# Kernel tuning notes

Measured on AMD Instinct MI355X. Metric: run time of the kernel, lower is better.

The kernel has to match this reference:

```python
import jax, jax.numpy as jnp
import numpy as np

B, T, V, E, H, L = 64, 512, 50000, 256, 256, 9


def _lstm_dir(x, w_ih, w_hh, b, reverse):
    # x: [B,T,I]; w_ih: [4H,I]; w_hh: [4H,H]; b: [4H]. PyTorch gate order i,f,g,o.
    Bm, Hm = x.shape[0], w_hh.shape[1]
    gx = jnp.einsum('bti,gi->btg', x, w_ih) + b  # [B,T,4H] precomputed input proj

    def step(carry, g_t):
        h, c = carry
        gates = g_t + h @ w_hh.T
        i, f, g, o = jnp.split(gates, 4, axis=-1)
        c = jax.nn.sigmoid(f) * c + jax.nn.sigmoid(i) * jnp.tanh(g)
        h = jax.nn.sigmoid(o) * jnp.tanh(c)
        return (h, c), h

    init = (jnp.zeros((Bm, Hm), x.dtype), jnp.zeros((Bm, Hm), x.dtype))
    _, hs = jax.lax.scan(step, init, jnp.swapaxes(gx, 0, 1), reverse=reverse)
    return jnp.swapaxes(hs, 0, 1)  # [B,T,H]


def _bilstm_layer(x, w_ih, w_hh, b):
    fwd = _lstm_dir(x, w_ih[0], w_hh[0], b[0], False)
    bwd = _lstm_dir(x, w_ih[1], w_hh[1], b[1], True)
    return jnp.concatenate([fwd, bwd], axis=-1)  # [B,T,2H]


def _crf_nll(emissions, labels, mask, trans, start_trans, end_trans):
    # emissions: [B,T,L]; labels: [B,T] int; mask: [B,T] (mask[:,0] assumed 1)
    maskf = mask.astype(emissions.dtype)
    # gold path score
    em_lab = jnp.take_along_axis(emissions, labels[..., None], axis=2)[..., 0]  # [B,T]
    trans_sc = trans[labels[:, :-1], labels[:, 1:]]  # [B,T-1]
    score = start_trans[labels[:, 0]] + em_lab[:, 0] \
        + jnp.sum((trans_sc + em_lab[:, 1:]) * maskf[:, 1:], axis=1)
    last_idx = jnp.sum(mask, axis=1).astype(jnp.int32) - 1
    last_lab = jnp.take_along_axis(labels, last_idx[:, None].astype(labels.dtype), axis=1)[:, 0]
    score = score + end_trans[last_lab]
    # log-partition via forward algorithm (scan over time)
    alpha0 = start_trans[None, :] + emissions[:, 0]  # [B,L]

    def step(alpha, xs):
        em_t, m_t = xs
        new = jax.nn.logsumexp(alpha[:, :, None] + trans[None], axis=1) + em_t
        alpha = jnp.where(m_t[:, None] > 0, new, alpha)
        return alpha, None

    alpha, _ = jax.lax.scan(
        step, alpha0,
        (jnp.swapaxes(emissions[:, 1:], 0, 1), jnp.swapaxes(mask[:, 1:], 0, 1)))
    logZ = jax.nn.logsumexp(alpha + end_trans[None, :], axis=1)  # [B]
    return -(score - logZ).mean()


def setup_inputs() -> dict:
    key = jax.random.key(0)
    ks = jax.random.split(key, 16)
    s = 0.05
    inp = {
        'input_ids': jax.random.randint(ks[0], (B, T), 0, V),
        'attention_mask': jnp.ones((B, T), jnp.int32),
        'labels': jax.random.randint(ks[1], (B, T), 0, L),
        'emb': jax.random.normal(ks[2], (V, E), jnp.float32) * s,
        # layer 0: input size E; layer 1: input size 2H. [dir, 4H, in]
        'w_ih0': jax.random.normal(ks[3], (2, 4 * H, E), jnp.float32) * s,
        'w_hh0': jax.random.normal(ks[4], (2, 4 * H, H), jnp.float32) * s,
        'b0': jax.random.normal(ks[5], (2, 4 * H), jnp.float32) * s,
        'w_ih1': jax.random.normal(ks[6], (2, 4 * H, 2 * H), jnp.float32) * s,
        'w_hh1': jax.random.normal(ks[7], (2, 4 * H, H), jnp.float32) * s,
        'b1': jax.random.normal(ks[8], (2, 4 * H), jnp.float32) * s,
        'lin_w': jax.random.normal(ks[9], (L, 2 * H), jnp.float32) * s,
        'lin_b': jax.random.normal(ks[10], (L,), jnp.float32) * s,
        'trans': jax.random.normal(ks[11], (L, L), jnp.float32) * 0.1,
        'start_trans': jax.random.normal(ks[12], (L,), jnp.float32) * 0.1,
        'end_trans': jax.random.normal(ks[13], (L,), jnp.float32) * 0.1,
    }
    return inp


def reference(input_ids, attention_mask, labels, emb, w_ih0, w_hh0, b0,
              w_ih1, w_hh1, b1, lin_w, lin_b, trans, start_trans, end_trans):
    x = emb[input_ids]                       # [B,T,E]
    x = _bilstm_layer(x, w_ih0, w_hh0, b0)   # [B,T,2H]
    x = _bilstm_layer(x, w_ih1, w_hh1, b1)   # [B,T,2H]
    emissions = x @ lin_w.T + lin_b          # [B,T,L]
    loss = _crf_nll(emissions, labels, attention_mask, trans, start_trans, end_trans)
    return loss
```

## Files before the change

### kernel.cpp

```cpp
#include <hip/hip_runtime.h>
#include <stdint.h>
#include <stddef.h>

#define B_ 64
#define T_ 512
#define E_ 256
#define H_ 256
#define L_ 9
#define BT (B_*T_)
#define G4 1024
#define N2 2048

typedef short    bf16x8  __attribute__((ext_vector_type(8)));
typedef float    f32x4   __attribute__((ext_vector_type(4)));
typedef int      i32x8   __attribute__((ext_vector_type(8)));

__device__ __forceinline__ unsigned short f2bf(float x){
    unsigned u = __builtin_bit_cast(unsigned, x);
    u += 0x7fffu + ((u >> 16) & 1u);
    return (unsigned short)(u >> 16);
}
__device__ __forceinline__ float bf2f(unsigned short h){
    unsigned u = ((unsigned)h) << 16;
    return __builtin_bit_cast(float, u);
}

__device__ __forceinline__ unsigned char f32_e4m3(float x){
    unsigned b = __builtin_bit_cast(unsigned, x);
    unsigned s = b >> 31;
    float a = fabsf(x);
    if (a >= 448.f) return (unsigned char)((s<<7) | 0x7E);
    int E = (int)((b>>23)&255) - 127;
    if (E < -6) E = -6;
    int qi = (int)rintf(a * exp2f((float)(3 - E)));
    if (qi >= 16){ qi >>= 1; ++E; }
    if (qi == 0) return (unsigned char)(s<<7);
    unsigned mag = (qi >= 8) ? ((((unsigned)(E + 7)) << 3) | (unsigned)(qi - 8))
                             : (unsigned)qi;
    return (unsigned char)((s<<7) | mag);
}

__device__ __forceinline__ float sigm(float x){
    return __builtin_amdgcn_rcpf(1.f + __expf(-x));
}
__device__ __forceinline__ float tanh_(float x){
    float e = __expf(2.f*x);
    return 1.f - 2.f*__builtin_amdgcn_rcpf(e + 1.f);
}

__device__ __forceinline__ void lds_load16(void* lds, const void* g){
    __builtin_amdgcn_global_load_lds(
        (const __attribute__((address_space(1))) void*)g,
        (__attribute__((address_space(3))) void*)lds, 16, 0, 0);
}

__device__ __forceinline__ void store_out(unsigned short* p, float v){ *p = f2bf(v); }
__device__ __forceinline__ void store_out(float* p, float v){ *p = v; }

__global__ void k_embed(const int* __restrict__ ids, const float* __restrict__ emb,
                        unsigned short* __restrict__ x0){
    int bt = blockIdx.x;
    int e  = threadIdx.x;
    int id = ids[bt];
    x0[(size_t)bt*E_ + e] = f2bf(emb[(size_t)id*E_ + e]);
}

__global__ void k_pack_wih(const float* __restrict__ in, unsigned short* __restrict__ out, int K){
    int p = blockIdx.y;
    int k = blockIdx.x*256 + threadIdx.x;
    int dirc = p >> 10, pp = p & 1023;
    int wv = pp >> 7, rem = pp & 127;
    int uh = (rem >> 6) & 1, g = (rem >> 4) & 3, ulx = rem & 15;
    int orig = dirc*1024 + g*256 + wv*32 + uh*16 + ulx;
    out[(size_t)p*K + k] = f2bf(in[(size_t)orig*K + k]);
}

__global__ void k_pack_bias(const float* __restrict__ b, float* __restrict__ bp){
    int p = blockIdx.x*256 + threadIdx.x;
    int dirc = p >> 10, pp = p & 1023;
    int wv = pp >> 7, rem = pp & 127;
    int uh = (rem >> 6) & 1, g = (rem >> 4) & 3, ulx = rem & 15;
    int orig = dirc*1024 + g*256 + wv*32 + uh*16 + ulx;
    bp[p] = b[orig];
}

__global__ void k_pack_wfp8(const float* __restrict__ whh, unsigned char* __restrict__ wpk){
    int idx = blockIdx.x*256 + threadIdx.x;
    int lane = idx & 63;
    int uh   = (idx >> 6) & 1;
    int g    = (idx >> 7) & 3;
    int kt   = (idx >> 9) & 1;
    int wv   = (idx >> 10) & 7;
    int dir  = (idx >> 13) & 1;
    int ulx = lane & 15, hi4 = lane >> 4;
    int row = g*256 + wv*32 + uh*16 + ulx;
    int k0 = kt*128 + hi4*32;
    const float* src = whh + ((size_t)dir*G4 + row)*H_ + k0;
    unsigned char* dst = wpk + (size_t)idx*32;
    #pragma unroll
    for (int q = 0; q < 32; ++q) dst[q] = f32_e4m3(src[q]);
}

__global__ __launch_bounds__(256) void k_gemm(const unsigned short* __restrict__ A,
                                              const unsigned short* __restrict__ Bm,
                                              const float* __restrict__ bias,
                                              unsigned short* __restrict__ C,
                                              int M, int N, int K){
    __shared__ unsigned short As[128*32];
    __shared__ unsigned short Bs[128*32];
    int tid = threadIdx.x, lane = tid & 63, w = tid >> 6;
    int wm = w >> 1, wn = w & 1;
    int tileM = blockIdx.y * 128, tileN = blockIdx.x * 128;
    f32x4 acc[4][4] = {};
    const char* Ab = (const char*)A;
    const char* Bb = (const char*)Bm;
    for (int k0 = 0; k0 < K; k0 += 32){
        #pragma unroll
        for (int i = 0; i < 2; ++i){
            int off = (w*2 + i)*1024 + lane*16;
            int row = off >> 6, colb = off & 63;
            lds_load16((char*)As + (w*2+i)*1024,
                       Ab + ((size_t)(tileM + row)*K + k0)*2 + colb);
            lds_load16((char*)Bs + (w*2+i)*1024,
                       Bb + ((size_t)(tileN + row)*K + k0)*2 + colb);
        }
        __syncthreads();
        int kloc = (lane >> 4) * 8;
        bf16x8 af[4], bfv[4];
        #pragma unroll
        for (int mf = 0; mf < 4; ++mf)
            af[mf] = *(const bf16x8*)&As[(wm*64 + mf*16 + (lane & 15))*32 + kloc];
        #pragma unroll
        for (int nf = 0; nf < 4; ++nf)
            bfv[nf] = *(const bf16x8*)&Bs[(wn*64 + nf*16 + (lane & 15))*32 + kloc];
        #pragma unroll
        for (int mf = 0; mf < 4; ++mf)
            #pragma unroll
            for (int nf = 0; nf < 4; ++nf)
                acc[mf][nf] = __builtin_amdgcn_mfma_f32_16x16x32_bf16(
                                  af[mf], bfv[nf], acc[mf][nf], 0, 0, 0);
        __syncthreads();
    }
    #pragma unroll
    for (int mf = 0; mf < 4; ++mf){
        #pragma unroll
        for (int nf = 0; nf < 4; ++nf){
            int row0 = tileM + wm*64 + mf*16 + (lane >> 4)*4;
            int col  = tileN + wn*64 + nf*16 + (lane & 15);
            float bv = bias[col];
            #pragma unroll
            for (int r = 0; r < 4; ++r)
                C[(size_t)(row0 + r)*N + col] = f2bf(acc[mf][nf][r] + bv);
        }
    }
}

template<typename OutT>
__global__ __launch_bounds__(512, 2)
void k_rec_mfma(const unsigned short* __restrict__ gx,
                const unsigned char* __restrict__ wpk,
                OutT* __restrict__ out){
    int blk = blockIdx.x;
    int dir = blk & 1, bg = blk >> 1;
    int tid = threadIdx.x, lane = tid & 63, w = tid >> 6;
    int ul = lane & 15, hi4 = lane >> 4;
    int batch = bg*4 + hi4;

    __shared__ __align__(16) unsigned char hlds[2][32][16][8];
    {
        unsigned long long* hz = (unsigned long long*)hlds;
        for (int i = tid; i < 1024; i += 512) hz[i] = 0ull;
    }

    i32x8 wf[2][4][2];
    {
        const i32x8* wb = (const i32x8*)wpk;
        #pragma unroll
        for (int kt = 0; kt < 2; ++kt)
            #pragma unroll
            for (int g = 0; g < 4; ++g)
                #pragma unroll
                for (int uh = 0; uh < 2; ++uh)
                    wf[kt][g][uh] = wb[((((size_t)(dir*8 + w)*2 + kt)*4 + g)*2 + uh)*64 + lane];
    }
    __syncthreads();

    const unsigned short* gp = gx + (size_t)(batch*T_ + (dir ? T_-1 : 0))*N2
                                  + dir*1024 + w*128 + ul;
    ptrdiff_t dstep = dir ? -(ptrdiff_t)N2 : (ptrdiff_t)N2;

    unsigned short gxr[8];
    #pragma unroll
    for (int uh = 0; uh < 2; ++uh)
        #pragma unroll
        for (int g = 0; g < 4; ++g)
            gxr[uh*4+g] = gp[uh*64 + g*16];

    float c0 = 0.f, c1 = 0.f;
    int u0 = w*32 + ul, u1 = u0 + 16;
    OutT* ob = out + (size_t)batch*T_*512 + dir*256;

    for (int s = 0; s < T_; ++s){
        int buf = s & 1;
        f32x4 acc[4][2];
        #pragma unroll
        for (int g = 0; g < 4; ++g)
            #pragma unroll
            for (int uh = 0; uh < 2; ++uh)
                acc[g][uh] = (f32x4){ bf2f(gxr[uh*4+g]), 0.f, 0.f, 0.f };

        gp += dstep;
        unsigned short gxn[8];
        #pragma unroll
        for (int uh = 0; uh < 2; ++uh)
            #pragma unroll
            for (int g = 0; g < 4; ++g)
                gxn[uh*4+g] = gp[uh*64 + g*16];

        const unsigned long long* hrow = (const unsigned long long*)&hlds[buf][0][0][0];
        #pragma unroll
        for (int kt = 0; kt < 2; ++kt){
            unsigned long long a0 = hrow[(kt*16 + hi4*4 + 0)*16 + ul];
            unsigned long long a1 = hrow[(kt*16 + hi4*4 + 1)*16 + ul];
            unsigned long long a2 = hrow[(kt*16 + hi4*4 + 2)*16 + ul];
            unsigned long long a3 = hrow[(kt*16 + hi4*4 + 3)*16 + ul];
            i32x8 af = (i32x8){ (int)a0, (int)(a0>>32), (int)a1, (int)(a1>>32),
                                (int)a2, (int)(a2>>32), (int)a3, (int)(a3>>32) };
            #pragma unroll
            for (int g = 0; g < 4; ++g)
                #pragma unroll
                for (int uh = 0; uh < 2; ++uh)
                    acc[g][uh] = __builtin_amdgcn_mfma_scale_f32_16x16x128_f8f6f4(
                                     af, wf[kt][g][uh], acc[g][uh],
                                     0, 0,
                                     0, 0x7f7f7f7f,
                                     0, 0x7f7f7f7f);
        }

        int tt = dir ? (T_-1-s) : s;
        float h0, h1;
        {
            float xi = acc[0][0][0], xf = acc[1][0][0], xg = acc[2][0][0], xo = acc[3][0][0];
            c0 = sigm(xf)*c0 + sigm(xi)*tanh_(xg);
            h0 = sigm(xo)*tanh_(c0);
        }
        {
            float xi = acc[0][1][0], xf = acc[1][1][0], xg = acc[2][1][0], xo = acc[3][1][0];
            c1 = sigm(xf)*c1 + sigm(xi)*tanh_(xg);
            h1 = sigm(xo)*tanh_(c1);
        }

        unsigned char hb0, hb1;
#if __has_builtin(__builtin_amdgcn_cvt_pk_fp8_f32)
        {
            int pk = __builtin_amdgcn_cvt_pk_fp8_f32(h0, h1, 0, false);
            hb0 = (unsigned char)(pk & 0xff);
            hb1 = (unsigned char)((pk >> 8) & 0xff);
        }
#else
        hb0 = f32_e4m3(h0); hb1 = f32_e4m3(h1);
#endif
        hlds[buf^1][u0>>3][hi4*4][u0&7] = hb0;
        hlds[buf^1][u1>>3][hi4*4][u1&7] = hb1;

        store_out(&ob[(size_t)tt*512 + u0], h0);
        store_out(&ob[(size_t)tt*512 + u1], h1);

        #pragma unroll
        for (int i = 0; i < 8; ++i) gxr[i] = gxn[i];
        __syncthreads();
    }
}

__global__ __launch_bounds__(256) void k_linear(const float* __restrict__ x,
                                                const float* __restrict__ w,
                                                const float* __restrict__ bias,
                                                float* __restrict__ em){
    int wv = threadIdx.x >> 6, lane = threadIdx.x & 63;
    int bt = blockIdx.x*4 + wv;
    const float4* xp = (const float4*)(x + (size_t)bt*(2*H_) + lane*8);
    float4 xa = xp[0], xb = xp[1];
    #pragma unroll
    for (int l = 0; l < L_; ++l){
        const float4* wp = (const float4*)(w + (size_t)l*(2*H_) + lane*8);
        float4 wa = wp[0], wb = wp[1];
        float p = xa.x*wa.x + xa.y*wa.y + xa.z*wa.z + xa.w*wa.w
                + xb.x*wb.x + xb.y*wb.y + xb.z*wb.z + xb.w*wb.w;
        #pragma unroll
        for (int o = 32; o; o >>= 1) p += __shfl_xor(p, o);
        if (lane == 0) em[(size_t)bt*L_ + l] = p + bias[l];
    }
}

__global__ void k_crf(const float* __restrict__ em, const int* __restrict__ labels,
                      const int* __restrict__ mask, const float* __restrict__ trans,
                      const float* __restrict__ st, const float* __restrict__ et,
                      float* __restrict__ out){
    int b = blockIdx.x, lane = threadIdx.x;
    __shared__ float tr[L_*L_];
    for (int i = lane; i < L_*L_; i += 64) tr[i] = trans[i];
    __syncthreads();
    const float* e  = em + (size_t)b*T_*L_;
    const int* lab  = labels + b*T_;
    const int* mk   = mask + b*T_;
    float sc = 0.f; int msum = 0;
    for (int t = lane; t < T_; t += 64){
        msum += mk[t];
        if (t >= 1)
            sc += (tr[lab[t-1]*L_ + lab[t]] + e[t*L_ + lab[t]]) * (float)mk[t];
    }
    #pragma unroll
    for (int o = 32; o; o >>= 1){ sc += __shfl_xor(sc, o); msum += __shfl_xor(msum, o); }
    int lj = lane < L_ ? lane : 0;
    float alpha = (lane < L_) ? (st[lj] + e[lj]) : -3.0e38f;
    for (int t = 1; t < T_; ++t){
        float v[L_]; float m = -3.0e38f;
        #pragma unroll
        for (int i = 0; i < L_; ++i){
            float ai = __shfl(alpha, i);
            v[i] = ai + tr[i*L_ + lj];
            m = fmaxf(m, v[i]);
        }
        float ssum = 0.f;
        #pragma unroll
        for (int i = 0; i < L_; ++i) ssum += __expf(v[i] - m);
        float nw = m + __logf(ssum) + e[t*L_ + lj];
        if (lane < L_ && mk[t] > 0) alpha = nw;
    }
    float av = (lane < L_) ? alpha + et[lj] : -3.0e38f;
    float m2 = av;
    #pragma unroll
    for (int o = 32; o; o >>= 1) m2 = fmaxf(m2, __shfl_xor(m2, o));
    float s2 = (lane < L_) ? __expf(av - m2) : 0.f;
    #pragma unroll
    for (int o = 32; o; o >>= 1) s2 += __shfl_xor(s2, o);
    if (lane == 0){
        float logZ = m2 + __logf(s2);
        int last = msum - 1;
        float score = sc + st[lab[0]] + e[lab[0]] + et[lab[last]];
        atomicAdd(out, (logZ - score) * (1.f/(float)B_));
    }
}

extern "C" void kernel_launch(void* const* d_in, const int* in_sizes, int n_in,
                              void* d_out, int out_size, void* d_ws, size_t ws_size,
                              hipStream_t stream){
    (void)in_sizes; (void)n_in; (void)out_size; (void)ws_size;
    const int*   ids    = (const int*)d_in[0];
    const int*   amask  = (const int*)d_in[1];
    const int*   labels = (const int*)d_in[2];
    const float* emb    = (const float*)d_in[3];
    const float* w_ih0  = (const float*)d_in[4];
    const float* w_hh0  = (const float*)d_in[5];
    const float* b0     = (const float*)d_in[6];
    const float* w_ih1  = (const float*)d_in[7];
    const float* w_hh1  = (const float*)d_in[8];
    const float* b1     = (const float*)d_in[9];
    const float* lin_w  = (const float*)d_in[10];
    const float* lin_b  = (const float*)d_in[11];
    const float* trans  = (const float*)d_in[12];
    const float* st     = (const float*)d_in[13];
    const float* et     = (const float*)d_in[14];
    float* out = (float*)d_out;

    char* ws = (char*)d_ws;
    size_t o = 0;
    auto alloc = [&](size_t bytes)->char*{
        char* p = ws + o; o = (o + bytes + 255) & ~(size_t)255; return p;
    };
    unsigned short* x0    = (unsigned short*)alloc((size_t)BT*E_*2);
    unsigned short* wih0p = (unsigned short*)alloc((size_t)N2*E_*2);
    unsigned short* wih1p = (unsigned short*)alloc((size_t)N2*512*2);
    unsigned char*  wpk0  = (unsigned char*)alloc(16384*32);
    unsigned char*  wpk1  = (unsigned char*)alloc(16384*32);
    float*          bp0   = (float*)alloc(N2*4);
    float*          bp1   = (float*)alloc(N2*4);
    unsigned short* gx    = (unsigned short*)alloc((size_t)BT*N2*2);
    unsigned short* xc1   = (unsigned short*)alloc((size_t)BT*512*2);
    float*          xc2   = (float*)alloc((size_t)BT*512*4);
    float*          em    = (float*)alloc((size_t)BT*L_*4 + 1024);

    hipMemsetAsync(d_out, 0, sizeof(float), stream);

    k_pack_wih<<<dim3(E_/256, N2), 256, 0, stream>>>(w_ih0, wih0p, E_);
    k_pack_wih<<<dim3(512/256, N2), 256, 0, stream>>>(w_ih1, wih1p, 512);
    k_pack_bias<<<N2/256, 256, 0, stream>>>(b0, bp0);
    k_pack_bias<<<N2/256, 256, 0, stream>>>(b1, bp1);
    k_pack_wfp8<<<16384/256, 256, 0, stream>>>(w_hh0, wpk0);
    k_pack_wfp8<<<16384/256, 256, 0, stream>>>(w_hh1, wpk1);
    k_embed<<<BT, E_, 0, stream>>>(ids, emb, x0);

    k_gemm<<<dim3(N2/128, BT/128), 256, 0, stream>>>(x0, wih0p, bp0, gx, BT, N2, E_);
    k_rec_mfma<unsigned short><<<32, 512, 0, stream>>>(gx, wpk0, xc1);
    k_gemm<<<dim3(N2/128, BT/128), 256, 0, stream>>>(xc1, wih1p, bp1, gx, BT, N2, 512);
    k_rec_mfma<float><<<32, 512, 0, stream>>>(gx, wpk1, xc2);

    k_linear<<<BT/4, 256, 0, stream>>>(xc2, lin_w, lin_b, em);
    k_crf<<<B_, 64, 0, stream>>>(em, labels, amask, trans, st, et, out);
}
```

Before: 1.358 ms.

## Switch input-projection GEMMs to FP8 MFMA with swizzled LDS tiles

Embeddings, input weights and the layer-1 hidden output are now stored as FP8 e4m3 instead of bf16. The input-projection GEMM uses the 16x16x128 scaled FP8 MFMA with a K=128 tile and an XOR-swizzled LDS layout. This halves operand bandwidth and cuts the number of MFMA instructions and K-loop iterations. The recurrent kernel writes its FP8 hidden bytes directly for layer 1, and a lighter LDS-only barrier replaces __syncthreads in both kernels. The cost is lower precision in the input projections, and the barrier relies on no outstanding global memory ops needing to complete at that point.

```diff
diff --git a/kernel.cpp b/kernel.cpp
--- a/kernel.cpp
+++ b/kernel.cpp
@@ -13,6 +13,7 @@
 
 typedef short    bf16x8  __attribute__((ext_vector_type(8)));
 typedef float    f32x4   __attribute__((ext_vector_type(4)));
+typedef int      i32x4   __attribute__((ext_vector_type(4)));
 typedef int      i32x8   __attribute__((ext_vector_type(8)));
 
 __device__ __forceinline__ unsigned short f2bf(float x){
@@ -54,25 +55,31 @@
         (__attribute__((address_space(3))) void*)lds, 16, 0, 0);
 }
 
+__device__ __forceinline__ void barrier_lds(){
+    asm volatile("s_waitcnt lgkmcnt(0)" ::: "memory");
+    __builtin_amdgcn_s_barrier();
+    __builtin_amdgcn_sched_barrier(0);
+}
+
 __device__ __forceinline__ void store_out(unsigned short* p, float v){ *p = f2bf(v); }
 __device__ __forceinline__ void store_out(float* p, float v){ *p = v; }
 
 __global__ void k_embed(const int* __restrict__ ids, const float* __restrict__ emb,
-                        unsigned short* __restrict__ x0){
+                        unsigned char* __restrict__ x0){
     int bt = blockIdx.x;
     int e  = threadIdx.x;
     int id = ids[bt];
-    x0[(size_t)bt*E_ + e] = f2bf(emb[(size_t)id*E_ + e]);
-}
-
-__global__ void k_pack_wih(const float* __restrict__ in, unsigned short* __restrict__ out, int K){
+    x0[(size_t)bt*E_ + e] = f32_e4m3(emb[(size_t)id*E_ + e]);
+}
+
+__global__ void k_pack_wih(const float* __restrict__ in, unsigned char* __restrict__ out, int K){
     int p = blockIdx.y;
     int k = blockIdx.x*256 + threadIdx.x;
     int dirc = p >> 10, pp = p & 1023;
     int wv = pp >> 7, rem = pp & 127;
     int uh = (rem >> 6) & 1, g = (rem >> 4) & 3, ulx = rem & 15;
     int orig = dirc*1024 + g*256 + wv*32 + uh*16 + ulx;
-    out[(size_t)p*K + k] = f2bf(in[(size_t)orig*K + k]);
+    out[(size_t)p*K + k] = f32_e4m3(in[(size_t)orig*K + k]);
 }
 
 __global__ void k_pack_bias(const float* __restrict__ b, float* __restrict__ bp){
@@ -101,45 +108,53 @@
     for (int q = 0; q < 32; ++q) dst[q] = f32_e4m3(src[q]);
 }
 
-__global__ __launch_bounds__(256) void k_gemm(const unsigned short* __restrict__ A,
-                                              const unsigned short* __restrict__ Bm,
-                                              const float* __restrict__ bias,
-                                              unsigned short* __restrict__ C,
-                                              int M, int N, int K){
-    __shared__ unsigned short As[128*32];
-    __shared__ unsigned short Bs[128*32];
+__global__ __launch_bounds__(256) void k_gemm_fp8(const unsigned char* __restrict__ A,
+                                                  const unsigned char* __restrict__ Bm,
+                                                  const float* __restrict__ bias,
+                                                  unsigned short* __restrict__ C,
+                                                  int M, int N, int K){
+    __shared__ __align__(16) unsigned char As[16384];
+    __shared__ __align__(16) unsigned char Bs[16384];
     int tid = threadIdx.x, lane = tid & 63, w = tid >> 6;
     int wm = w >> 1, wn = w & 1;
     int tileM = blockIdx.y * 128, tileN = blockIdx.x * 128;
     f32x4 acc[4][4] = {};
-    const char* Ab = (const char*)A;
-    const char* Bb = (const char*)Bm;
-    for (int k0 = 0; k0 < K; k0 += 32){
-        #pragma unroll
-        for (int i = 0; i < 2; ++i){
-            int off = (w*2 + i)*1024 + lane*16;
-            int row = off >> 6, colb = off & 63;
-            lds_load16((char*)As + (w*2+i)*1024,
-                       Ab + ((size_t)(tileM + row)*K + k0)*2 + colb);
-            lds_load16((char*)Bs + (w*2+i)*1024,
-                       Bb + ((size_t)(tileN + row)*K + k0)*2 + colb);
+    for (int k0 = 0; k0 < K; k0 += 128){
+        #pragma unroll
+        for (int p = 0; p < 4; ++p){
+            int idx = (p*256 + tid)*16;
+            int ks = idx >> 12, rem = idx & 4095, row = rem >> 5;
+            int jsrc = (rem & 16) ^ ((row & 4) << 2);
+            lds_load16((char*)As + idx, A + (size_t)(tileM + row)*K + k0 + ks*32 + jsrc);
+            lds_load16((char*)Bs + idx, Bm + (size_t)(tileN + row)*K + k0 + ks*32 + jsrc);
         }
         __syncthreads();
-        int kloc = (lane >> 4) * 8;
-        bf16x8 af[4], bfv[4];
+        int ks = lane >> 4, m15 = lane & 15;
+        i32x8 af[4], bfv[4];
+        #pragma unroll
+        for (int mf = 0; mf < 4; ++mf){
+            int r = wm*64 + mf*16 + m15;
+            int base = ks*4096 + r*32, sw = (r & 4) << 2;
+            i32x4 lo = *(const i32x4*)((const char*)As + base + sw);
+            i32x4 hi = *(const i32x4*)((const char*)As + base + (16 ^ sw));
+            af[mf] = __builtin_shufflevector(lo, hi, 0,1,2,3,4,5,6,7);
+        }
+        #pragma unroll
+        for (int nf = 0; nf < 4; ++nf){
+            int r = wn*64 + nf*16 + m15;
+            int base = ks*4096 + r*32, sw = (r & 4) << 2;
+            i32x4 lo = *(const i32x4*)((const char*)Bs + base + sw);
+            i32x4 hi = *(const i32x4*)((const char*)Bs + base + (16 ^ sw));
+            bfv[nf] = __builtin_shufflevector(lo, hi, 0,1,2,3,4,5,6,7);
+        }
         #pragma unroll
         for (int mf = 0; mf < 4; ++mf)
-            af[mf] = *(const bf16x8*)&As[(wm*64 + mf*16 + (lane & 15))*32 + kloc];
-        #pragma unroll
-        for (int nf = 0; nf < 4; ++nf)
-            bfv[nf] = *(const bf16x8*)&Bs[(wn*64 + nf*16 + (lane & 15))*32 + kloc];
-        #pragma unroll
-        for (int mf = 0; mf < 4; ++mf)
             #pragma unroll
             for (int nf = 0; nf < 4; ++nf)
-                acc[mf][nf] = __builtin_amdgcn_mfma_f32_16x16x32_bf16(
-                                  af[mf], bfv[nf], acc[mf][nf], 0, 0, 0);
-        __syncthreads();
+                acc[mf][nf] = __builtin_amdgcn_mfma_scale_f32_16x16x128_f8f6f4(
+                                  af[mf], bfv[nf], acc[mf][nf],
+                                  0, 0, 0, 0x7f7f7f7f, 0, 0x7f7f7f7f);
+        barrier_lds();
     }
     #pragma unroll
     for (int mf = 0; mf < 4; ++mf){
@@ -232,9 +247,7 @@
                 for (int uh = 0; uh < 2; ++uh)
                     acc[g][uh] = __builtin_amdgcn_mfma_scale_f32_16x16x128_f8f6f4(
                                      af, wf[kt][g][uh], acc[g][uh],
-                                     0, 0,
-                                     0, 0x7f7f7f7f,
-                                     0, 0x7f7f7f7f);
+                                     0, 0, 0, 0x7f7f7f7f, 0, 0x7f7f7f7f);
         }
 
         int tt = dir ? (T_-1-s) : s;
@@ -263,12 +276,17 @@
         hlds[buf^1][u0>>3][hi4*4][u0&7] = hb0;
         hlds[buf^1][u1>>3][hi4*4][u1&7] = hb1;
 
-        store_out(&ob[(size_t)tt*512 + u0], h0);
-        store_out(&ob[(size_t)tt*512 + u1], h1);
+        if constexpr (sizeof(OutT) == 1){
+            ((unsigned char*)ob)[(size_t)tt*512 + u0] = hb0;
+            ((unsigned char*)ob)[(size_t)tt*512 + u1] = hb1;
+        } else {
+            store_out(&ob[(size_t)tt*512 + u0], h0);
+            store_out(&ob[(size_t)tt*512 + u1], h1);
+        }
 
         #pragma unroll
         for (int i = 0; i < 8; ++i) gxr[i] = gxn[i];
-        __syncthreads();
+        barrier_lds();
     }
 }
 
@@ -368,15 +386,15 @@
     auto alloc = [&](size_t bytes)->char*{
         char* p = ws + o; o = (o + bytes + 255) & ~(size_t)255; return p;
     };
-    unsigned short* x0    = (unsigned short*)alloc((size_t)BT*E_*2);
-    unsigned short* wih0p = (unsigned short*)alloc((size_t)N2*E_*2);
-    unsigned short* wih1p = (unsigned short*)alloc((size_t)N2*512*2);
+    unsigned char*  x0    = (unsigned char*)alloc((size_t)BT*E_);
+    unsigned char*  wih0p = (unsigned char*)alloc((size_t)N2*E_);
+    unsigned char*  wih1p = (unsigned char*)alloc((size_t)N2*512);
     unsigned char*  wpk0  = (unsigned char*)alloc(16384*32);
     unsigned char*  wpk1  = (unsigned char*)alloc(16384*32);
     float*          bp0   = (float*)alloc(N2*4);
     float*          bp1   = (float*)alloc(N2*4);
     unsigned short* gx    = (unsigned short*)alloc((size_t)BT*N2*2);
-    unsigned short* xc1   = (unsigned short*)alloc((size_t)BT*512*2);
+    unsigned char*  xc1   = (unsigned char*)alloc((size_t)BT*512);
     float*          xc2   = (float*)alloc((size_t)BT*512*4);
     float*          em    = (float*)alloc((size_t)BT*L_*4 + 1024);
 
@@ -390,9 +408,9 @@
     k_pack_wfp8<<<16384/256, 256, 0, stream>>>(w_hh1, wpk1);
     k_embed<<<BT, E_, 0, stream>>>(ids, emb, x0);
 
-    k_gemm<<<dim3(N2/128, BT/128), 256, 0, stream>>>(x0, wih0p, bp0, gx, BT, N2, E_);
-    k_rec_mfma<unsigned short><<<32, 512, 0, stream>>>(gx, wpk0, xc1);
-    k_gemm<<<dim3(N2/128, BT/128), 256, 0, stream>>>(xc1, wih1p, bp1, gx, BT, N2, 512);
+    k_gemm_fp8<<<dim3(N2/128, BT/128), 256, 0, stream>>>(x0, wih0p, bp0, gx, BT, N2, E_);
+    k_rec_mfma<unsigned char><<<32, 512, 0, stream>>>(gx, wpk0, xc1);
+    k_gemm_fp8<<<dim3(N2/128, BT/128), 256, 0, stream>>>(xc1, wih1p, bp1, gx, BT, N2, 512);
     k_rec_mfma<float><<<32, 512, 0, stream>>>(gx, wpk1, xc2);
 
     k_linear<<<BT/4, 256, 0, stream>>>(xc2, lin_w, lin_b, em);
```

New measurement: 1.317 ms. -3.1%, faster.
